# Performance work log

Hardware: AMD Instinct MI355X
Metric: run time of the kernel (lower is better)

Reference implementation:

```python
import jax, jax.numpy as jnp
import numpy as np

D_MODEL = 1024
N_HEADS = 16
ORDER = 6          # P
P2 = 2 * ORDER - 1 # 11 collapsed Chebyshev terms
EPS_CLAMP = 1e-6
EPS_DEN = 1e-7


def _beta_np():
    # alpha_j = (j+1)^{-1.5}, j = 0..P-1
    j = np.arange(ORDER, dtype=np.float32)
    alpha = (j + 1.0) ** (-1.5)
    tail = np.flip(np.cumsum(np.flip(alpha)))  # tail[i] = sum_{j>=i} alpha_j
    beta = np.concatenate([np.zeros(1, np.float32), tail[1:].astype(np.float32), np.zeros(ORDER - 1, np.float32)])
    return beta / beta.sum()


def _cheb(x):
    T = [jnp.ones_like(x), x]
    for _ in range(2, P2):
        T.append(2.0 * x * T[-1] - T[-2])
    return jnp.stack(T, axis=3)


def setup_inputs() -> dict:
    key = jax.random.key(0)
    k1, k2, k3 = jax.random.split(key, 3)
    B, S, D = 2, 1024, D_MODEL
    x = jax.random.normal(k1, (B, S, D), dtype=jnp.float32)
    W_in = jax.random.normal(k2, (3 * D, D), dtype=jnp.float32) * 0.02
    W_out = jax.random.normal(k3, (D, D), dtype=jnp.float32) * 0.02
    return {"x": x, "W_in": W_in, "W_out": W_out}


def reference(x, W_in, W_out):
    B, S, D = x.shape
    H, Dh = N_HEADS, D // N_HEADS

    # fused QKV projection (Linear, no bias): y = x @ W_in^T
    qkv = jnp.einsum('bsd,ed->bse', x, W_in)
    q, k, v = jnp.split(qkv, 3, axis=-1)
    # (B,S,H,Dh) -> (B,H,S,Dh)
    q = q.reshape(B, S, H, Dh).transpose(0, 2, 1, 3)
    k = k.reshape(B, S, H, Dh).transpose(0, 2, 1, 3)
    v = v.reshape(B, S, H, Dh).transpose(0, 2, 1, 3)

    inv_sqrt_d = 1.0 / jnp.sqrt(jnp.float32(Dh))
    xq = jnp.clip(q * inv_sqrt_d, -1.0 + EPS_CLAMP, 1.0 - EPS_CLAMP)
    xk = jnp.clip(k * inv_sqrt_d, -1.0 + EPS_CLAMP, 1.0 - EPS_CLAMP)

    Tq = _cheb(xq)  # (B,H,S,P2,Dh)
    Tk = _cheb(xk)  # (B,H,S,P2,Dh)

    beta = jnp.asarray(_beta_np())  # (P2,), same for all heads (fixed buffer)

    # causal prefix sums over sequence dim
    Tv = Tk * v[:, :, :, None, :]             # (B,H,S,P2,Dh)
    kv_prefix = jnp.cumsum(Tv, axis=2)        # (B,H,S,P2,Dh)
    ks_prefix = jnp.cumsum(Tk.sum(axis=-1), axis=2)  # (B,H,S,P2)

    kv_beta = kv_prefix * beta[None, None, None, :, None]
    k_beta = ks_prefix * beta[None, None, None, :]

    num = (Tq * kv_beta).sum(axis=3)                 # (B,H,S,Dh)
    den = (Tq.sum(axis=-1) * k_beta).sum(axis=3)     # (B,H,S)   den_normalization='none'

    out_h = num / (den[..., None] + EPS_DEN)
    out = out_h.transpose(0, 2, 1, 3).reshape(B, S, H * Dh)
    return jnp.einsum('bsd,ed->bse', out, W_out)
```

## Files before the change

### kernel.cpp

```cpp
#include <hip/hip_runtime.h>
#include <hip/hip_bf16.h>
#include <cstddef>
#include <cstdint>

#define BATCH 2
#define SEQ   1024
#define DMODEL 1024
#define NHEADS 16
#define DHEAD 64
#define E3D   3072
#define NCHUNK 64
#define CHUNK 16

#define BETA1 0.45736626f
#define BETA2 0.26218724f
#define BETA3 0.15594524f
#define BETA4 0.08693904f
#define BETA5 0.03756222f

#define RSCALE 2048.f
#define RINV   4.8828125e-4f

typedef __attribute__((ext_vector_type(8))) _Float16 half8;
typedef __attribute__((ext_vector_type(4))) float floatx4;

__device__ __forceinline__ void cp16(const void* g, void* l) {
    __builtin_amdgcn_global_load_lds(
        (const __attribute__((address_space(1))) void*)(uintptr_t)g,
        (__attribute__((address_space(3))) void*)(uintptr_t)l,
        16, 0, 0);
}

__device__ __forceinline__ void split2(float x, unsigned short* H, unsigned short* M) {
    _Float16 h = (_Float16)x;
    float r = (x - (float)h) * RSCALE;
    _Float16 m = (_Float16)r;
    *H = __builtin_bit_cast(unsigned short, h);
    *M = __builtin_bit_cast(unsigned short, m);
}

__device__ __forceinline__ void split2x4(const float4 v,
                                         unsigned short* h, unsigned short* m,
                                         size_t i4) {
    float vv[4] = {v.x, v.y, v.z, v.w};
    unsigned short hh[4], mm[4];
#pragma unroll
    for (int j = 0; j < 4; j++) split2(vv[j], &hh[j], &mm[j]);
    ((ushort4*)h)[i4] = make_ushort4(hh[0], hh[1], hh[2], hh[3]);
    ((ushort4*)m)[i4] = make_ushort4(mm[0], mm[1], mm[2], mm[3]);
}

__device__ __forceinline__ void cheb5(float x, float T[6]) {
    T[0] = 1.f; T[1] = x;
    float tx2 = 2.f * x;
    T[2] = tx2 * T[1] - T[0];
    T[3] = tx2 * T[2] - T[1];
    T[4] = tx2 * T[3] - T[2];
    T[5] = tx2 * T[4] - T[3];
}

__device__ __forceinline__ float clampx(float v) {
    return fminf(fmaxf(v * 0.125f, -1.f + 1e-6f), 1.f - 1e-6f);
}

__device__ __forceinline__ float wave_sum(float x) {
#pragma unroll
    for (int m = 32; m >= 1; m >>= 1) x += __shfl_xor(x, m, 64);
    return x;
}

__global__ __launch_bounds__(256) void k_splitall(
    const float* __restrict__ x, const float* __restrict__ Win,
    unsigned short* __restrict__ Xh, unsigned short* __restrict__ Xm,
    unsigned short* __restrict__ Wh, unsigned short* __restrict__ Wm)
{
    const float* in; unsigned short *h, *m; int i;
    if (blockIdx.x < 2048) {
        in = x; h = Xh; m = Xm;
        i = blockIdx.x * 256 + threadIdx.x;
    } else {
        in = Win; h = Wh; m = Wm;
        i = (blockIdx.x - 2048) * 256 + threadIdx.x;
    }
    split2x4(((const float4*)in)[i], h, m, i);
}

template<int TM>
__global__ __launch_bounds__(256, 3) void gemm_f16s(
    const unsigned short* __restrict__ Ah, const unsigned short* __restrict__ Am,
    const unsigned short* __restrict__ Bh, const unsigned short* __restrict__ Bm,
    float* __restrict__ C, int M, int N, int K)
{
    constexpr int ASZ = TM * 32;
    constexpr int BSZ = 128 * 32;
    constexpr int MT  = (TM >= 64) ? TM / 32 : 1;
    __shared__ unsigned short lds[2 * ASZ + 2 * BSZ];

    const int tid  = threadIdx.x;
    const int w    = tid >> 6;
    const int lane = tid & 63;
    const int m0 = blockIdx.y * TM;
    const int n0 = blockIdx.x * 128;

    const int rB0 = w * 32 + (lane >> 2);
    const int rB1 = rB0 + 16;
    const int sB0 = (lane & 3) ^ ((rB0 >> 1) & 3);
    const int sB1 = (lane & 3) ^ ((rB1 >> 1) & 3);
    const size_t offB0 = (size_t)(n0 + rB0) * K + sB0 * 8;
    const size_t offB1 = (size_t)(n0 + rB1) * K + sB1 * 8;
    const int ldsB0 = (w * 32) * 32;
    const int ldsB1 = (w * 32 + 16) * 32;

    const int rA0 = (TM >= 64) ? (w * (TM / 4) + (lane >> 2))
                               : (w * 16 + (lane >> 2));
    const int sA0 = (lane & 3) ^ ((rA0 >> 1) & 3);
    const size_t offA0 = (size_t)(m0 + rA0) * K + sA0 * 8;
    const int ldsA0 = ((TM >= 64) ? (w * (TM / 4)) : (w * 16)) * 32;
    const bool doA = (TM >= 64) || (w < 2);

    const int q = lane >> 4, l16 = lane & 15;
    const int wm = w & 1, wn = w >> 1;
    const int ra = wm * (TM / 2) + l16;
    const int rb = wn * 64 + l16;
    const int aadr = ra * 32 + ((q ^ ((ra >> 1) & 3)) * 8);
    const int badr = rb * 32 + ((q ^ ((rb >> 1) & 3)) * 8);

    floatx4 acc1[MT][4] = {};
    floatx4 acc2[MT][4] = {};

    for (int k0 = 0; k0 < K; k0 += 32) {
        __syncthreads();
        if (doA) {
            cp16(Ah + offA0 + k0, &lds[0 * ASZ + ldsA0]);
            cp16(Am + offA0 + k0, &lds[1 * ASZ + ldsA0]);
        }
        cp16(Bh + offB0 + k0, &lds[2 * ASZ + 0 * BSZ + ldsB0]);
        cp16(Bh + offB1 + k0, &lds[2 * ASZ + 0 * BSZ + ldsB1]);
        cp16(Bm + offB0 + k0, &lds[2 * ASZ + 1 * BSZ + ldsB0]);
        cp16(Bm + offB1 + k0, &lds[2 * ASZ + 1 * BSZ + ldsB1]);
        __syncthreads();

        half8 fah[MT], fam[MT], fbh[4], fbm[4];
#pragma unroll
        for (int t = 0; t < MT; t++) {
            fah[t] = *(const half8*)&lds[0 * ASZ + aadr + t * 512];
            fam[t] = *(const half8*)&lds[1 * ASZ + aadr + t * 512];
        }
#pragma unroll
        for (int t = 0; t < 4; t++) {
            fbh[t] = *(const half8*)&lds[2 * ASZ + 0 * BSZ + badr + t * 512];
            fbm[t] = *(const half8*)&lds[2 * ASZ + 1 * BSZ + badr + t * 512];
        }
#pragma unroll
        for (int mt = 0; mt < MT; mt++)
#pragma unroll
            for (int nt = 0; nt < 4; nt++) {
                acc1[mt][nt] = __builtin_amdgcn_mfma_f32_16x16x32_f16(
                    fah[mt], fbh[nt], acc1[mt][nt], 0, 0, 0);
                acc2[mt][nt] = __builtin_amdgcn_mfma_f32_16x16x32_f16(
                    fah[mt], fbm[nt], acc2[mt][nt], 0, 0, 0);
                acc2[mt][nt] = __builtin_amdgcn_mfma_f32_16x16x32_f16(
                    fam[mt], fbh[nt], acc2[mt][nt], 0, 0, 0);
            }
    }

#pragma unroll
    for (int mt = 0; mt < MT; mt++) {
        const int row0 = m0 + wm * (TM / 2) + mt * 16 + q * 4;
#pragma unroll
        for (int nt = 0; nt < 4; nt++) {
            const int col = n0 + wn * 64 + nt * 16 + l16;
#pragma unroll
            for (int r = 0; r < 4; r++)
                C[(size_t)(row0 + r) * N + col] = acc1[mt][nt][r] + acc2[mt][nt][r] * RINV;
        }
    }
}

__global__ __launch_bounds__(256) void k_mid(
    const float* __restrict__ Wout,
    unsigned short* __restrict__ Wouth, unsigned short* __restrict__ Woutm,
    const float* __restrict__ qkv,
    float* __restrict__ SQB, float* __restrict__ SK, float* __restrict__ KVC)
{
    const int blk = blockIdx.x;
    if (blk < 1024) {
        int i = blk * 256 + threadIdx.x;
        split2x4(((const float4*)Wout)[i], Wouth, Woutm, i);
        return;
    }
    if (blk < 9216) {
        const int lane = threadIdx.x & 63;
        const int pos  = (blk - 1024) * 4 + (threadIdx.x >> 6);
        const int bh = pos >> 10, s = pos & 1023;
        const int b = bh >> 4, h = bh & 15;
        const float* base = qkv + (size_t)(b * SEQ + s) * E3D + h * DHEAD + lane;
        float xq = clampx(base[0]);
        float xk = clampx(base[1024]);
        float Tq[6], Tk[6];
        cheb5(xq, Tq); cheb5(xk, Tk);
        const float BETA[5] = {BETA1, BETA2, BETA3, BETA4, BETA5};
#pragma unroll
        for (int p = 1; p <= 5; p++) {
            float sq = wave_sum(Tq[p]);
            float sk = wave_sum(Tk[p]);
            if (lane == 0) {
                SQB[(size_t)pos * 5 + p - 1] = sq * BETA[p - 1];
                SK[(size_t)pos * 5 + p - 1]  = sk;
            }
        }
        return;
    }
    {
        const int lane = threadIdx.x & 63;
        const int cid = (blk - 9216) * 4 + (threadIdx.x >> 6);
        const int bh = cid >> 6, chunk = cid & 63;
        const int b = bh >> 4, h = bh & 15;
        const float* kb = qkv + (size_t)(b * SEQ + chunk * CHUNK) * E3D + 1024 + h * DHEAD + lane;
        float kv[5] = {0.f, 0.f, 0.f, 0.f, 0.f};
#pragma unroll
        for (int i = 0; i < CHUNK; i++) {
            const float* row = kb + (size_t)i * E3D;
            float xk = clampx(row[0]);
            float v = row[1024];
            float T[6]; cheb5(xk, T);
#pragma unroll
            for (int p = 1; p <= 5; p++) kv[p - 1] += T[p] * v;
        }
#pragma unroll
        for (int p = 0; p < 5; p++) KVC[((size_t)cid * 5 + p) * 64 + lane] = kv[p];
    }
}

__global__ __launch_bounds__(320) void k_prefix(float* __restrict__ KVC,
                                                const float* __restrict__ SK,
                                                float* __restrict__ SKP)
{
    __shared__ float csum[NCHUNK * 5];
    const int bh = blockIdx.x;
    const int t = threadIdx.x;
    float v[NCHUNK];
    const size_t base = (size_t)bh * NCHUNK * 320 + t;
#pragma unroll
    for (int c = 0; c < NCHUNK; c++) v[c] = KVC[base + (size_t)c * 320];
    float run = 0.f;
#pragma unroll
    for (int c = 0; c < NCHUNK; c++) {
        KVC[base + (size_t)c * 320] = run;
        run += v[c];
    }
    {
        const int chunk = t / 5, p = t % 5;
        const float* sb = SK + ((size_t)bh * SEQ + chunk * CHUNK) * 5 + p;
        float s = 0.f;
#pragma unroll
        for (int i = 0; i < CHUNK; i++) s += sb[i * 5];
        csum[chunk * 5 + p] = s;
    }
    __syncthreads();
    if (t < 5) {
        float run2 = 0.f;
        for (int c = 0; c < NCHUNK; c++) {
            SKP[((size_t)bh * NCHUNK + c) * 5 + t] = run2;
            run2 += csum[c * 5 + t];
        }
    }
}

__global__ __launch_bounds__(256) void k_out(const float* __restrict__ qkv,
                                             const float* __restrict__ KVC,
                                             const float* __restrict__ SK,
                                             const float* __restrict__ SKP,
                                             const float* __restrict__ SQB,
                                             unsigned short* __restrict__ OH,
                                             unsigned short* __restrict__ OM)
{
    const int lane = threadIdx.x & 63;
    const int cid = blockIdx.x * 4 + (threadIdx.x >> 6);
    const int bh = cid >> 6, chunk = cid & 63;
    const int b = bh >> 4, h = bh & 15;
    const float BETA[5] = {BETA1, BETA2, BETA3, BETA4, BETA5};

    const int li = lane & 15;
    const int pos = bh * SEQ + chunk * CHUNK + li;
    float den_r = 0.f;
#pragma unroll
    for (int p = 0; p < 5; p++) {
        float v = SK[(size_t)pos * 5 + p];
#pragma unroll
        for (int off = 1; off < 16; off <<= 1) {
            float n = __shfl_up(v, off, 64);
            if (li >= off) v += n;
        }
        den_r += SQB[(size_t)pos * 5 + p] * (SKP[((size_t)bh * NCHUNK + chunk) * 5 + p] + v);
    }

    float kv[5];
#pragma unroll
    for (int p = 0; p < 5; p++) kv[p] = KVC[((size_t)cid * 5 + p) * 64 + lane];

    const float* qb = qkv + (size_t)(b * SEQ + chunk * CHUNK) * E3D + h * DHEAD + lane;
    size_t obase = (size_t)(b * SEQ + chunk * CHUNK) * DMODEL + h * DHEAD + lane;
#pragma unroll
    for (int i = 0; i < CHUNK; i++) {
        const float* row = qb + (size_t)i * E3D;
        float xq = clampx(row[0]);
        float xk = clampx(row[1024]);
        float v = row[2048];
        float Tk_[6]; cheb5(xk, Tk_);
#pragma unroll
        for (int p = 1; p <= 5; p++) kv[p - 1] += Tk_[p] * v;
        float Tq_[6]; cheb5(xq, Tq_);
        float num = 0.f;
#pragma unroll
        for (int p = 1; p <= 5; p++) num += BETA[p - 1] * Tq_[p] * kv[p - 1];
        float d = __shfl(den_r, i, 64);
        float val = num / (d + 1e-7f);
        unsigned short hh, mm;
        split2(val, &hh, &mm);
        size_t oi = obase + (size_t)i * DMODEL;
        OH[oi] = hh; OM[oi] = mm;
    }
}


extern "C" void kernel_launch(void* const* d_in, const int* in_sizes, int n_in,
                              void* d_out, int out_size, void* d_ws, size_t ws_size,
                              hipStream_t stream)
{
    const float* x    = (const float*)d_in[0];
    const float* Win  = (const float*)d_in[1];
    const float* Wout = (const float*)d_in[2];
    float* out = (float*)d_out;
    char* ws = (char*)d_ws;

    float* QKV = (float*)(ws + 0);
    unsigned short* Xh   = (unsigned short*)(ws + 25165824);
    unsigned short* Xm   = (unsigned short*)(ws + 29360128);
    unsigned short* Winh = (unsigned short*)(ws + 33554432);
    unsigned short* Winm = (unsigned short*)(ws + 39845888);
    float* SQB = (float*)(ws + 25165824);
    float* SK  = (float*)(ws + 25821184);
    float* SKP = (float*)(ws + 26476544);
    float* KVC = (float*)(ws + 26517504);
    unsigned short* OHh   = (unsigned short*)(ws + 33554432);
    unsigned short* OHm   = (unsigned short*)(ws + 37748736);
    unsigned short* Wouth = (unsigned short*)(ws + 41943040);
    unsigned short* Woutm = (unsigned short*)(ws + 44040192);

    k_splitall<<<5120, 256, 0, stream>>>(x, Win, Xh, Xm, Winh, Winm);

    gemm_f16s<64><<<dim3(24, 32), 256, 0, stream>>>(Xh, Xm, Winh, Winm,
                                                    QKV, BATCH * SEQ, E3D, DMODEL);

    k_mid<<<9728, 256, 0, stream>>>(Wout, Wouth, Woutm, QKV, SQB, SK, KVC);

    k_prefix<<<BATCH * NHEADS, 320, 0, stream>>>(KVC, SK, SKP);

    k_out<<<512, 256, 0, stream>>>(QKV, KVC, SK, SKP, SQB, OHh, OHm);

    gemm_f16s<32><<<dim3(8, 64), 256, 0, stream>>>(OHh, OHm, Wouth, Woutm,
                                                   out, BATCH * SEQ, DMODEL, DMODEL);
}
```

Baseline: 181.1 us.

## Switch split-fp16 GEMMs to 32x32x16 MFMA with retuned tiles

Replaces the 16x16x32 MFMA GEMM with a variant built on 32x32x16 MFMA instructions. Each wave computes 32-row by TN/2-column tiles, and the QKV and output projections are retiled (64x192 and 64x64 blocks, both on a 16x32 grid). The larger MFMA shape is meant to cut LDS fragment reads per flop and raise matrix-unit efficiency. In exchange it uses more accumulator registers, so occupancy is limited to 2 blocks per SM, and the output projection runs with smaller tiles.

```diff
diff --git a/kernel.cpp b/kernel.cpp
--- a/kernel.cpp
+++ b/kernel.cpp
@@ -22,7 +22,7 @@
 #define RINV   4.8828125e-4f
 
 typedef __attribute__((ext_vector_type(8))) _Float16 half8;
-typedef __attribute__((ext_vector_type(4))) float floatx4;
+typedef __attribute__((ext_vector_type(16))) float floatx16;
 
 __device__ __forceinline__ void cp16(const void* g, void* l) {
     __builtin_amdgcn_global_load_lds(
@@ -85,94 +85,91 @@
     split2x4(((const float4*)in)[i], h, m, i);
 }
 
-template<int TM>
-__global__ __launch_bounds__(256, 3) void gemm_f16s(
+template<int TN>
+__global__ __launch_bounds__(256, 2) void gemm_w32(
     const unsigned short* __restrict__ Ah, const unsigned short* __restrict__ Am,
     const unsigned short* __restrict__ Bh, const unsigned short* __restrict__ Bm,
     float* __restrict__ C, int M, int N, int K)
 {
-    constexpr int ASZ = TM * 32;
-    constexpr int BSZ = 128 * 32;
-    constexpr int MT  = (TM >= 64) ? TM / 32 : 1;
+    constexpr int NT  = TN / 64;
+    constexpr int ASZ = 64 * 32;
+    constexpr int BSZ = TN * 32;
     __shared__ unsigned short lds[2 * ASZ + 2 * BSZ];
 
     const int tid  = threadIdx.x;
     const int w    = tid >> 6;
     const int lane = tid & 63;
-    const int m0 = blockIdx.y * TM;
-    const int n0 = blockIdx.x * 128;
-
-    const int rB0 = w * 32 + (lane >> 2);
-    const int rB1 = rB0 + 16;
-    const int sB0 = (lane & 3) ^ ((rB0 >> 1) & 3);
-    const int sB1 = (lane & 3) ^ ((rB1 >> 1) & 3);
-    const size_t offB0 = (size_t)(n0 + rB0) * K + sB0 * 8;
-    const size_t offB1 = (size_t)(n0 + rB1) * K + sB1 * 8;
-    const int ldsB0 = (w * 32) * 32;
-    const int ldsB1 = (w * 32 + 16) * 32;
-
-    const int rA0 = (TM >= 64) ? (w * (TM / 4) + (lane >> 2))
-                               : (w * 16 + (lane >> 2));
-    const int sA0 = (lane & 3) ^ ((rA0 >> 1) & 3);
-    const size_t offA0 = (size_t)(m0 + rA0) * K + sA0 * 8;
-    const int ldsA0 = ((TM >= 64) ? (w * (TM / 4)) : (w * 16)) * 32;
-    const bool doA = (TM >= 64) || (w < 2);
-
-    const int q = lane >> 4, l16 = lane & 15;
+    const int m0 = blockIdx.y * 64;
+    const int n0 = blockIdx.x * TN;
+
+    const int arow = w * 16 + (lane >> 2);
+    const int asg  = (lane & 3) ^ ((arow >> 1) & 3);
+    const size_t offA = (size_t)(m0 + arow) * K + asg * 8;
+    const int ldsA = (w * 16) * 32;
+    size_t offB[NT];
+    int ldsB[NT];
+#pragma unroll
+    for (int j = 0; j < NT; j++) {
+        const int brow = j * 64 + w * 16 + (lane >> 2);
+        const int bsg  = (lane & 3) ^ ((brow >> 1) & 3);
+        offB[j] = (size_t)(n0 + brow) * K + bsg * 8;
+        ldsB[j] = (j * 64 + w * 16) * 32;
+    }
+
+    const int l32 = lane & 31, q32 = lane >> 5;
     const int wm = w & 1, wn = w >> 1;
-    const int ra = wm * (TM / 2) + l16;
-    const int rb = wn * 64 + l16;
-    const int aadr = ra * 32 + ((q ^ ((ra >> 1) & 3)) * 8);
-    const int badr = rb * 32 + ((q ^ ((rb >> 1) & 3)) * 8);
-
-    floatx4 acc1[MT][4] = {};
-    floatx4 acc2[MT][4] = {};
+    const int ra = wm * 32 + l32;
+    const int abase = ra * 32, aswz = (ra >> 1) & 3;
+    int bbase[NT], bswz[NT];
+#pragma unroll
+    for (int nt = 0; nt < NT; nt++) {
+        const int rb = wn * (TN / 2) + nt * 32 + l32;
+        bbase[nt] = rb * 32;
+        bswz[nt] = (rb >> 1) & 3;
+    }
+
+    floatx16 acc1[NT] = {};
+    floatx16 acc2[NT] = {};
 
     for (int k0 = 0; k0 < K; k0 += 32) {
         __syncthreads();
-        if (doA) {
-            cp16(Ah + offA0 + k0, &lds[0 * ASZ + ldsA0]);
-            cp16(Am + offA0 + k0, &lds[1 * ASZ + ldsA0]);
-        }
-        cp16(Bh + offB0 + k0, &lds[2 * ASZ + 0 * BSZ + ldsB0]);
-        cp16(Bh + offB1 + k0, &lds[2 * ASZ + 0 * BSZ + ldsB1]);
-        cp16(Bm + offB0 + k0, &lds[2 * ASZ + 1 * BSZ + ldsB0]);
-        cp16(Bm + offB1 + k0, &lds[2 * ASZ + 1 * BSZ + ldsB1]);
+        cp16(Ah + offA + k0, &lds[ldsA]);
+        cp16(Am + offA + k0, &lds[ASZ + ldsA]);
+#pragma unroll
+        for (int j = 0; j < NT; j++) {
+            cp16(Bh + offB[j] + k0, &lds[2 * ASZ + ldsB[j]]);
+            cp16(Bm + offB[j] + k0, &lds[2 * ASZ + BSZ + ldsB[j]]);
+        }
         __syncthreads();
 
-        half8 fah[MT], fam[MT], fbh[4], fbm[4];
-#pragma unroll
-        for (int t = 0; t < MT; t++) {
-            fah[t] = *(const half8*)&lds[0 * ASZ + aadr + t * 512];
-            fam[t] = *(const half8*)&lds[1 * ASZ + aadr + t * 512];
-        }
-#pragma unroll
-        for (int t = 0; t < 4; t++) {
-            fbh[t] = *(const half8*)&lds[2 * ASZ + 0 * BSZ + badr + t * 512];
-            fbm[t] = *(const half8*)&lds[2 * ASZ + 1 * BSZ + badr + t * 512];
-        }
-#pragma unroll
-        for (int mt = 0; mt < MT; mt++)
-#pragma unroll
-            for (int nt = 0; nt < 4; nt++) {
-                acc1[mt][nt] = __builtin_amdgcn_mfma_f32_16x16x32_f16(
-                    fah[mt], fbh[nt], acc1[mt][nt], 0, 0, 0);
-                acc2[mt][nt] = __builtin_amdgcn_mfma_f32_16x16x32_f16(
-                    fah[mt], fbm[nt], acc2[mt][nt], 0, 0, 0);
-                acc2[mt][nt] = __builtin_amdgcn_mfma_f32_16x16x32_f16(
-                    fam[mt], fbh[nt], acc2[mt][nt], 0, 0, 0);
+#pragma unroll
+        for (int kk = 0; kk < 2; kk++) {
+            const int ksel = kk * 2 + q32;
+            half8 fah = *(const half8*)&lds[abase + ((ksel ^ aswz) * 8)];
+            half8 fam = *(const half8*)&lds[ASZ + abase + ((ksel ^ aswz) * 8)];
+            half8 fbh[NT], fbm[NT];
+#pragma unroll
+            for (int nt = 0; nt < NT; nt++) {
+                fbh[nt] = *(const half8*)&lds[2 * ASZ + bbase[nt] + ((ksel ^ bswz[nt]) * 8)];
+                fbm[nt] = *(const half8*)&lds[2 * ASZ + BSZ + bbase[nt] + ((ksel ^ bswz[nt]) * 8)];
             }
-    }
-
-#pragma unroll
-    for (int mt = 0; mt < MT; mt++) {
-        const int row0 = m0 + wm * (TM / 2) + mt * 16 + q * 4;
-#pragma unroll
-        for (int nt = 0; nt < 4; nt++) {
-            const int col = n0 + wn * 64 + nt * 16 + l16;
-#pragma unroll
-            for (int r = 0; r < 4; r++)
-                C[(size_t)(row0 + r) * N + col] = acc1[mt][nt][r] + acc2[mt][nt][r] * RINV;
+#pragma unroll
+            for (int nt = 0; nt < NT; nt++) {
+                acc1[nt] = __builtin_amdgcn_mfma_f32_32x32x16_f16(fah, fbh[nt], acc1[nt], 0, 0, 0);
+                acc2[nt] = __builtin_amdgcn_mfma_f32_32x32x16_f16(fah, fbm[nt], acc2[nt], 0, 0, 0);
+                acc2[nt] = __builtin_amdgcn_mfma_f32_32x32x16_f16(fam, fbh[nt], acc2[nt], 0, 0, 0);
+            }
+        }
+    }
+
+    const int r0 = m0 + wm * 32 + q32 * 4;
+#pragma unroll
+    for (int nt = 0; nt < NT; nt++) {
+        const int c0 = n0 + wn * (TN / 2) + nt * 32 + l32;
+#pragma unroll
+        for (int reg = 0; reg < 16; reg++) {
+            const int row = r0 + (reg & 3) + 8 * (reg >> 2);
+            C[(size_t)row * N + c0] = acc1[nt][reg] + acc2[nt][reg] * RINV;
         }
     }
 }
@@ -350,7 +347,7 @@
 
     k_splitall<<<5120, 256, 0, stream>>>(x, Win, Xh, Xm, Winh, Winm);
 
-    gemm_f16s<64><<<dim3(24, 32), 256, 0, stream>>>(Xh, Xm, Winh, Winm,
+    gemm_w32<192><<<dim3(16, 32), 256, 0, stream>>>(Xh, Xm, Winh, Winm,
                                                     QKV, BATCH * SEQ, E3D, DMODEL);
 
     k_mid<<<9728, 256, 0, stream>>>(Wout, Wouth, Woutm, QKV, SQB, SK, KVC);
@@ -359,6 +356,6 @@
 
     k_out<<<512, 256, 0, stream>>>(QKV, KVC, SK, SKP, SQB, OHh, OHm);
 
-    gemm_f16s<32><<<dim3(8, 64), 256, 0, stream>>>(OHh, OHm, Wouth, Woutm,
+    gemm_w32<64><<<dim3(16, 32), 256, 0, stream>>>(OHh, OHm, Wouth, Woutm,
                                                    out, BATCH * SEQ, DMODEL, DMODEL);
 }
```

Result: no change. 179.7 us (-0.8%).
